# Kernel optimization log

Measured on AMD Instinct MI355X. Metric: run time of the kernel, lower is better.

## Reference

```python
import jax, jax.numpy as jnp
import numpy as np

N_NODES = 50000
N_EDGES = 640000
IN_DIM = 128
HID = 256
OUT = 256
BN_EPS = 1e-5
L2_EPS = 1e-12


def setup_inputs() -> dict:
    key = jax.random.key(0)
    ks = jax.random.split(key, 12)
    x = jax.random.normal(ks[0], (N_NODES, IN_DIM), dtype=jnp.float32)
    edge_index = jax.random.randint(ks[1], (2, N_EDGES), 0, N_NODES, dtype=jnp.int64)
    s0 = 1.0 / np.sqrt(IN_DIM)
    s1 = 1.0 / np.sqrt(HID)
    return {
        "x": x,
        "edge_index": edge_index,
        # SAGEConv layer 0: lin_l (aggregated neighbors, with bias), lin_r (root, no bias)
        "W_l0": jax.random.uniform(ks[2], (IN_DIM, HID), jnp.float32, -s0, s0),
        "b_l0": jax.random.uniform(ks[3], (HID,), jnp.float32, -s0, s0),
        "W_r0": jax.random.uniform(ks[4], (IN_DIM, HID), jnp.float32, -s0, s0),
        # SAGEConv layer 1
        "W_l1": jax.random.uniform(ks[5], (HID, OUT), jnp.float32, -s1, s1),
        "b_l1": jax.random.uniform(ks[6], (OUT,), jnp.float32, -s1, s1),
        "W_r1": jax.random.uniform(ks[7], (HID, OUT), jnp.float32, -s1, s1),
        # BatchNorm1d (eval mode: running stats)
        "bn_gamma": jax.random.uniform(ks[8], (HID,), jnp.float32, 0.5, 1.5),
        "bn_beta": 0.1 * jax.random.normal(ks[9], (HID,), dtype=jnp.float32),
        "bn_mean": 0.1 * jax.random.normal(ks[10], (HID,), dtype=jnp.float32),
        "bn_var": jax.random.uniform(ks[11], (HID,), jnp.float32, 0.5, 1.5),
    }


def _l2norm(v):
    # F.normalize(v, p=2, dim=1)
    n = jnp.sqrt(jnp.sum(v * v, axis=1, keepdims=True))
    return v / jnp.maximum(n, L2_EPS)


def _sage_mean(x, src, dst, W_l, b_l, W_r, n_nodes):
    # mean-aggregate source features at destination nodes (PyG source_to_target)
    msg = x[src]                                   # [E, d] gather
    agg = jax.ops.segment_sum(msg, dst, num_segments=n_nodes)
    cnt = jax.ops.segment_sum(jnp.ones((src.shape[0], 1), x.dtype), dst, num_segments=n_nodes)
    agg = agg / jnp.maximum(cnt, 1.0)
    out = agg @ W_l + b_l + x @ W_r
    return _l2norm(out)                            # SAGEConv(normalize=True)


def reference(x, edge_index, W_l0, b_l0, W_r0, W_l1, b_l1, W_r1,
              bn_gamma, bn_beta, bn_mean, bn_var):
    src, dst = edge_index[0], edge_index[1]
    n = x.shape[0]
    h = _sage_mean(x, src, dst, W_l0, b_l0, W_r0, n)
    # BatchNorm1d in eval mode (dropout is identity in eval)
    h = (h - bn_mean) * (bn_gamma / jnp.sqrt(bn_var + BN_EPS)) + bn_beta
    h = jax.nn.relu(h)
    h = _sage_mean(h, src, dst, W_l1, b_l1, W_r1, n)
    # final F.normalize(x, p=2, dim=1)
    return _l2norm(h)
```

## Files before the change

### kernel.cpp

```cpp
#include <hip/hip_runtime.h>

#define NN 50000

typedef __bf16 bf16x8 __attribute__((ext_vector_type(8)));
typedef float f32x4 __attribute__((ext_vector_type(4)));
typedef float f32x2 __attribute__((ext_vector_type(2)));

__device__ __forceinline__ unsigned short f2bf(float f) {
    unsigned int u = __builtin_bit_cast(unsigned int, f);
    u += 0x7FFF + ((u >> 16) & 1);
    return (unsigned short)(u >> 16);
}
__device__ __forceinline__ unsigned char f2fp8(float f) {
    return (unsigned char)(__builtin_amdgcn_cvt_pk_fp8_f32(f, f, 0, false) & 0xff);
}
__device__ __forceinline__ void gload16(const void* g, void* l) {
    __builtin_amdgcn_global_load_lds(
        (const __attribute__((address_space(1))) unsigned int*)g,
        (__attribute__((address_space(3))) unsigned int*)l, 16, 0, 0);
}

__global__ void init_kernel(const int* __restrict__ ei32, int* __restrict__ flag,
                            int* __restrict__ cnt, int n) {
    if (blockIdx.x == 0) {
        __shared__ int red[256];
        int tid = threadIdx.x;
        int o = 0;
        for (int i = tid; i < 4096; i += 256) o |= ei32[2 * i + 1];
        red[tid] = o;
        __syncthreads();
        for (int s = 128; s > 0; s >>= 1) {
            if (tid < s) red[tid] |= red[tid + s];
            __syncthreads();
        }
        if (tid == 0) *flag = (red[0] == 0) ? 1 : 0;
    } else {
        int i0 = (blockIdx.x - 1) * 1024 + threadIdx.x * 4;
#pragma unroll
        for (int j = 0; j < 4; ++j) {
            int i = i0 + j;
            if (i < n) cnt[i] = 0;
        }
    }
}

__device__ __forceinline__ int load_edge(const void* ei, int is64, long long idx) {
    return is64 ? (int)((const long long*)ei)[idx] : ((const int*)ei)[idx];
}

__global__ void hist_kernel(const void* __restrict__ ei, const int* __restrict__ flag,
                            int* __restrict__ cnt, unsigned short* __restrict__ rank, int E) {
    int e = blockIdx.x * blockDim.x + threadIdx.x;
    if (e >= E) return;
    int is64 = *flag;
    int dst = load_edge(ei, is64, (long long)E + e);
    int r = atomicAdd(&cnt[dst], 1);
    rank[e] = (unsigned short)r;
}

__global__ void scan_part(const int* __restrict__ cnt, int* __restrict__ bsum, int n) {
    __shared__ int s[256];
    const int tid = threadIdx.x;
    const int i0 = blockIdx.x * 1024 + tid * 4;
    int sum = 0;
#pragma unroll
    for (int j = 0; j < 4; ++j) {
        int i = i0 + j;
        if (i < n) sum += cnt[i];
    }
    s[tid] = sum;
    __syncthreads();
    for (int o = 128; o > 0; o >>= 1) {
        if (tid < o) s[tid] += s[tid + o];
        __syncthreads();
    }
    if (tid == 0) bsum[blockIdx.x] = s[0];
}

__global__ void scan_fin2(const int* __restrict__ cnt, const int* __restrict__ bsum,
                          int* __restrict__ off, int n, int nb) {
    __shared__ int s[256];
    __shared__ int base_sh, total_sh;
    const int tid = threadIdx.x;
    if (tid < 64) {
        int v = (tid < nb) ? bsum[tid] : 0;
        int incl = v;
#pragma unroll
        for (int o = 1; o < 64; o <<= 1) {
            int t = __shfl_up(incl, o, 64);
            if (tid >= o) incl += t;
        }
        if (tid == (int)blockIdx.x) base_sh = incl - v;
        if (tid == 63) total_sh = incl;
    }
    const int i0 = blockIdx.x * 1024 + tid * 4;
    int v[4];
    int sum = 0;
#pragma unroll
    for (int j = 0; j < 4; ++j) {
        int i = i0 + j;
        v[j] = (i < n) ? cnt[i] : 0;
        sum += v[j];
    }
    s[tid] = sum;
    __syncthreads();
    for (int o = 1; o < 256; o <<= 1) {
        int t = 0;
        if (tid >= o) t = s[tid - o];
        __syncthreads();
        s[tid] += t;
        __syncthreads();
    }
    int run = base_sh + s[tid] - sum;
#pragma unroll
    for (int j = 0; j < 4; ++j) {
        int i = i0 + j;
        if (i < n) {
            off[i] = run;
            run += v[j];
        }
    }
    if (blockIdx.x == 0 && tid == 0) off[n] = total_sh;
}

__global__ void fill_prep(const void* __restrict__ ei, const int* __restrict__ flag,
                          const int* __restrict__ off, const unsigned short* __restrict__ rank,
                          unsigned short* __restrict__ adj, int E, int EB,
                          const float* __restrict__ x, unsigned char* __restrict__ xf8,
                          unsigned short* __restrict__ xbf_t,
                          const float* __restrict__ Wl0, const float* __restrict__ Wr0,
                          unsigned short* __restrict__ Wt0,
                          const float* __restrict__ Wl1, const float* __restrict__ Wr1,
                          unsigned short* __restrict__ Wt1, int n4, int NC) {
    int b = blockIdx.x;
    if (b < EB) {
        int e = b * 256 + threadIdx.x;
        if (e >= E) return;
        int is64 = *flag;
        int src = load_edge(ei, is64, e);
        int dst = load_edge(ei, is64, (long long)E + e);
        int p = off[dst] + (int)rank[e];
        adj[p] = (unsigned short)src;
    } else if (b < EB + NC) {
        int i = (b - EB) * 256 + threadIdx.x;
        if (i >= n4) return;
        float4 v = ((const float4*)x)[i];
        int p8 = __builtin_amdgcn_cvt_pk_fp8_f32(v.x, v.y, 0, false);
        p8 = __builtin_amdgcn_cvt_pk_fp8_f32(v.z, v.w, p8, true);
        ((unsigned int*)xf8)[i] = (unsigned int)p8;
        uint2 o;
        o.x = (unsigned int)f2bf(v.x) | ((unsigned int)f2bf(v.y) << 16);
        o.y = (unsigned int)f2bf(v.z) | ((unsigned int)f2bf(v.w) << 16);
        int r = i >> 5;
        int kk = (i & 31) * 4;
        int ts = kk >> 5, q = (kk >> 3) & 3, e = kk & 7;
        size_t idx = ((size_t)(r >> 6) * 4 + ts) * 2048 + q * 512 + (r & 63) * 8 + e;
        *(uint2*)(xbf_t + idx) = o;
    } else if (b < EB + NC + 256) {
        int c = b - EB - NC;
        for (int k = threadIdx.x; k < 256; k += blockDim.x) {
            float v = (k < 128) ? Wl0[(size_t)k * 256 + c] : Wr0[(size_t)(k - 128) * 256 + c];
            int ks = k >> 5, q = (k >> 3) & 3, e = k & 7;
            Wt0[(size_t)ks * 8192 + q * 2048 + c * 8 + e] = f2bf(v);
        }
    } else {
        int c = b - EB - NC - 256;
        for (int k = threadIdx.x; k < 512; k += blockDim.x) {
            float v = (k < 256) ? Wl1[(size_t)k * 256 + c] : Wr1[(size_t)(k - 256) * 256 + c];
            int ks = k >> 5, q = (k >> 3) & 3, e = k & 7;
            Wt1[(size_t)ks * 8192 + q * 2048 + c * 8 + e] = f2bf(v);
        }
    }
}

__global__ void agg_l0(const unsigned char* __restrict__ feat8, const int* __restrict__ off,
                       const unsigned short* __restrict__ adj,
                       unsigned short* __restrict__ out_t, int n) {
    int node = blockIdx.x * 8 + (threadIdx.x >> 5);
    if (node >= n) return;
    const int lane = threadIdx.x & 31;
    const int s = off[node], e = off[node + 1];

    float a0[4] = {}, a1[4] = {}, a2[4] = {}, a3[4] = {};
    const unsigned char* fbase = feat8 + lane * 4;

    auto addrow = [&](float* acc, int src) {
        unsigned int u = *(const unsigned int*)(fbase + (size_t)src * 128);
        f32x2 lo = __builtin_amdgcn_cvt_pk_f32_fp8(u, false);
        f32x2 hi = __builtin_amdgcn_cvt_pk_f32_fp8(u, true);
        acc[0] += lo[0];
        acc[1] += lo[1];
        acc[2] += hi[0];
        acc[3] += hi[1];
    };

    int j = s;
    for (; j + 4 <= e; j += 4) {
        int i0 = adj[j], i1 = adj[j + 1], i2 = adj[j + 2], i3 = adj[j + 3];
        addrow(a0, i0);
        addrow(a1, i1);
        addrow(a2, i2);
        addrow(a3, i3);
    }
    {
        int rem = e - j;
        if (rem > 0) addrow(a0, adj[j]);
        if (rem > 1) addrow(a1, adj[j + 1]);
        if (rem > 2) addrow(a2, adj[j + 2]);
    }

    int deg = e - s;
    float inv = 1.0f / (float)(deg > 0 ? deg : 1);
#pragma unroll
    for (int k = 0; k < 4; ++k) a0[k] = (a0[k] + a1[k] + a2[k] + a3[k]) * inv;

    const int k0 = lane * 4;
    const int ts = k0 >> 5, q = (k0 >> 3) & 3, e8 = k0 & 7;
    size_t idx = ((size_t)(node >> 6) * 4 + ts) * 2048 + q * 512 + (node & 63) * 8 + e8;
    uint2 o;
    o.x = (unsigned int)f2bf(a0[0]) | ((unsigned int)f2bf(a0[1]) << 16);
    o.y = (unsigned int)f2bf(a0[2]) | ((unsigned int)f2bf(a0[3]) << 16);
    *(uint2*)(out_t + idx) = o;
}

__global__ void agg_l1(const unsigned char* __restrict__ feat8, const int* __restrict__ off,
                       const unsigned short* __restrict__ adj,
                       unsigned short* __restrict__ out_t, int n) {
    int node = blockIdx.x * 8 + (threadIdx.x >> 5);
    if (node >= n) return;
    const int lane = threadIdx.x & 31;
    const int s = off[node], e = off[node + 1];

    float a0[8] = {}, a1[8] = {}, a2[8] = {}, a3[8] = {};
    const unsigned char* fbase = feat8 + lane * 8;

    auto addrow = [&](float* acc, int src) {
        uint2 u = *(const uint2*)(fbase + (size_t)src * 256);
        f32x2 p0 = __builtin_amdgcn_cvt_pk_f32_fp8(u.x, false);
        f32x2 p1 = __builtin_amdgcn_cvt_pk_f32_fp8(u.x, true);
        f32x2 p2 = __builtin_amdgcn_cvt_pk_f32_fp8(u.y, false);
        f32x2 p3 = __builtin_amdgcn_cvt_pk_f32_fp8(u.y, true);
        acc[0] += p0[0];
        acc[1] += p0[1];
        acc[2] += p1[0];
        acc[3] += p1[1];
        acc[4] += p2[0];
        acc[5] += p2[1];
        acc[6] += p3[0];
        acc[7] += p3[1];
    };

    int j = s;
    for (; j + 4 <= e; j += 4) {
        int i0 = adj[j], i1 = adj[j + 1], i2 = adj[j + 2], i3 = adj[j + 3];
        addrow(a0, i0);
        addrow(a1, i1);
        addrow(a2, i2);
        addrow(a3, i3);
    }
    {
        int rem = e - j;
        if (rem > 0) addrow(a0, adj[j]);
        if (rem > 1) addrow(a1, adj[j + 1]);
        if (rem > 2) addrow(a2, adj[j + 2]);
    }

    int deg = e - s;
    float inv = 1.0f / (float)(deg > 0 ? deg : 1);
#pragma unroll
    for (int k = 0; k < 8; ++k) a0[k] = (a0[k] + a1[k] + a2[k] + a3[k]) * inv;

    const int k0 = lane * 8;
    const int ts = k0 >> 5, q = (k0 >> 3) & 3;
    size_t idx = ((size_t)(node >> 6) * 8 + ts) * 2048 + q * 512 + (node & 63) * 8;
    uint4 o;
    o.x = (unsigned int)f2bf(a0[0]) | ((unsigned int)f2bf(a0[1]) << 16);
    o.y = (unsigned int)f2bf(a0[2]) | ((unsigned int)f2bf(a0[3]) << 16);
    o.z = (unsigned int)f2bf(a0[4]) | ((unsigned int)f2bf(a0[5]) << 16);
    o.w = (unsigned int)f2bf(a0[6]) | ((unsigned int)f2bf(a0[7]) << 16);
    *(uint4*)(out_t + idx) = o;
}

template <int KH, bool L0>
__device__ __forceinline__ void sage_body(
    unsigned char (*a_sh)[4096], unsigned char (*b_sh)[16384],
    float (*red)[64], float* inv_sh,
    const unsigned short* __restrict__ Aagg_t, const unsigned short* __restrict__ Axin_t,
    const unsigned short* __restrict__ WtT, const float* __restrict__ bl,
    const float* __restrict__ bng, const float* __restrict__ bnb,
    const float* __restrict__ bnm, const float* __restrict__ bnv,
    unsigned char* __restrict__ hout8, unsigned short* __restrict__ hout_t,
    float* __restrict__ fout, int n) {
    constexpr int NSTEP = (2 * KH) / 32;
    constexpr int NAT = KH / 32;

    const int tid = threadIdx.x;
    const int w = tid >> 6;
    const int l = tid & 63;
    const int g = l >> 4;
    const int li = l & 15;
    const int row0 = blockIdx.x * 64;
    const int blk = blockIdx.x;

    f32x4 acc[4][4];
#pragma unroll
    for (int m = 0; m < 4; ++m)
#pragma unroll
        for (int nn = 0; nn < 4; ++nn) acc[m][nn] = (f32x4)(0.0f);

    auto stage = [&](int buf, int t) {
        const unsigned short* at =
            (t < NAT) ? Aagg_t + ((size_t)blk * NAT + t) * 2048
                      : Axin_t + ((size_t)blk * NAT + (t - NAT)) * 2048;
        gload16((const char*)at + w * 1024 + l * 16, &a_sh[buf][w * 1024]);
#pragma unroll
        for (int q = 0; q < 4; ++q)
            gload16((const char*)(WtT + (size_t)t * 8192) + q * 4096 + w * 1024 + l * 16,
                    &b_sh[buf][q * 4096 + w * 1024]);
    };

    auto compute = [&](int buf) {
        bf16x8 bfr[4];
#pragma unroll
        for (int nn = 0; nn < 4; ++nn)
            bfr[nn] = __builtin_bit_cast(
                bf16x8, *(const uint4*)&b_sh[buf][g * 4096 + (w * 64 + nn * 16 + li) * 16]);
        bf16x8 afr[4];
#pragma unroll
        for (int m = 0; m < 4; ++m)
            afr[m] = __builtin_bit_cast(bf16x8, *(const uint4*)&a_sh[buf][g * 1024 + (16 * m + li) * 16]);
#pragma unroll
        for (int nn = 0; nn < 4; ++nn)
#pragma unroll
            for (int m = 0; m < 4; ++m)
                acc[m][nn] = __builtin_amdgcn_mfma_f32_16x16x32_bf16(afr[m], bfr[nn], acc[m][nn], 0, 0, 0);
    };

    stage(0, 0);
    __syncthreads();

    int cur = 0;
    for (int ks = 0; ks < NSTEP - 1; ++ks) {
        stage(cur ^ 1, ks + 1);
        asm volatile("s_waitcnt vmcnt(5)" ::: "memory");
        __builtin_amdgcn_sched_barrier(0);
        __builtin_amdgcn_s_barrier();
        __builtin_amdgcn_sched_barrier(0);
        compute(cur);
        __builtin_amdgcn_s_barrier();
        __builtin_amdgcn_sched_barrier(0);
        cur ^= 1;
    }
    asm volatile("s_waitcnt vmcnt(0)" ::: "memory");
    __builtin_amdgcn_sched_barrier(0);
    __builtin_amdgcn_s_barrier();
    __builtin_amdgcn_sched_barrier(0);
    compute(cur);

    float bv[4];
#pragma unroll
    for (int nn = 0; nn < 4; ++nn) bv[nn] = bl[w * 64 + nn * 16 + li];
#pragma unroll
    for (int m = 0; m < 4; ++m)
#pragma unroll
        for (int nn = 0; nn < 4; ++nn)
#pragma unroll
            for (int r = 0; r < 4; ++r) acc[m][nn][r] += bv[nn];

    float ssp[4][4];
#pragma unroll
    for (int m = 0; m < 4; ++m)
#pragma unroll
        for (int r = 0; r < 4; ++r) {
            float s = 0.f;
#pragma unroll
            for (int nn = 0; nn < 4; ++nn) s += acc[m][nn][r] * acc[m][nn][r];
#pragma unroll
            for (int mk = 1; mk < 16; mk <<= 1) s += __shfl_xor(s, mk, 64);
            ssp[m][r] = s;
        }
    __syncthreads();
    if (li == 0) {
#pragma unroll
        for (int m = 0; m < 4; ++m)
#pragma unroll
            for (int r = 0; r < 4; ++r) red[w][16 * m + 4 * g + r] = ssp[m][r];
    }
    __syncthreads();
    if (tid < 64) {
        float tot = red[0][tid] + red[1][tid] + red[2][tid] + red[3][tid];
        inv_sh[tid] = 1.0f / fmaxf(sqrtf(tot), 1e-12f);
    }
    __syncthreads();

    float sc[4], sh[4];
    if (L0) {
#pragma unroll
        for (int nn = 0; nn < 4; ++nn) {
            int c = w * 64 + nn * 16 + li;
            float s = bng[c] * rsqrtf(bnv[c] + 1e-5f);
            sc[nn] = s;
            sh[nn] = bnb[c] - bnm[c] * s;
        }
    }
#pragma unroll
    for (int m = 0; m < 4; ++m) {
#pragma unroll
        for (int r = 0; r < 4; ++r) {
            int rl = 16 * m + 4 * g + r;
            int row = row0 + rl;
            if (row < n) {
                float inv = inv_sh[rl];
#pragma unroll
                for (int nn = 0; nn < 4; ++nn) {
                    int c = w * 64 + nn * 16 + li;
                    float v = acc[m][nn][r] * inv;
                    if (L0) {
                        v = fmaxf(v * sc[nn] + sh[nn], 0.f);
                        hout8[(size_t)row * 256 + c] = f2fp8(v);
                        int ts = c >> 5, q = (c >> 3) & 3, e8 = c & 7;
                        hout_t[((size_t)(row >> 6) * 8 + ts) * 2048 + q * 512 + (row & 63) * 8 + e8] =
                            f2bf(v);
                    } else {
                        fout[(size_t)row * 256 + c] = v;
                    }
                }
            }
        }
    }
}

__global__ void gemm_l0(const unsigned short* __restrict__ Aagg_t,
                        const unsigned short* __restrict__ Axin_t,
                        const unsigned short* __restrict__ WtT, const float* __restrict__ bl,
                        const float* __restrict__ bng, const float* __restrict__ bnb,
                        const float* __restrict__ bnm, const float* __restrict__ bnv,
                        unsigned char* __restrict__ hout8, unsigned short* __restrict__ hout_t,
                        int n) {
    __shared__ __align__(16) unsigned char a_sh[2][4096];
    __shared__ __align__(16) unsigned char b_sh[2][16384];
    __shared__ float red[4][64];
    __shared__ float inv_sh[64];
    sage_body<128, true>(a_sh, b_sh, red, inv_sh, Aagg_t, Axin_t, WtT, bl, bng, bnb, bnm, bnv,
                         hout8, hout_t, nullptr, n);
}

__global__ void gemm_l1(const unsigned short* __restrict__ Aagg_t,
                        const unsigned short* __restrict__ Axin_t,
                        const unsigned short* __restrict__ WtT, const float* __restrict__ bl,
                        float* __restrict__ fout, int n) {
    __shared__ __align__(16) unsigned char a_sh[2][4096];
    __shared__ __align__(16) unsigned char b_sh[2][16384];
    __shared__ float red[4][64];
    __shared__ float inv_sh[64];
    sage_body<256, false>(a_sh, b_sh, red, inv_sh, Aagg_t, Axin_t, WtT, bl, nullptr, nullptr,
                          nullptr, nullptr, nullptr, nullptr, fout, n);
}

extern "C" void kernel_launch(void* const* d_in, const int* in_sizes, int n_in,
                              void* d_out, int out_size, void* d_ws, size_t ws_size,
                              hipStream_t stream) {
    const float* x   = (const float*)d_in[0];
    const void*  ei  = d_in[1];
    const float* Wl0 = (const float*)d_in[2];
    const float* bl0 = (const float*)d_in[3];
    const float* Wr0 = (const float*)d_in[4];
    const float* Wl1 = (const float*)d_in[5];
    const float* bl1 = (const float*)d_in[6];
    const float* Wr1 = (const float*)d_in[7];
    const float* bng = (const float*)d_in[8];
    const float* bnb = (const float*)d_in[9];
    const float* bnm = (const float*)d_in[10];
    const float* bnv = (const float*)d_in[11];
    float* out = (float*)d_out;

    const int N = NN;
    const int E = in_sizes[1] / 2;
    const int NB = (N + 1023) / 1024;
    const int NBK = (N + 63) / 64;
    const int EB = (E + 255) / 256;

    char* wsp = (char*)d_ws;
    size_t o = 0;
    auto carve = [&](size_t bytes) {
        void* p = wsp + o;
        o = (o + bytes + 255) & ~(size_t)255;
        return p;
    };
    int* flag = (int*)carve(4);
    int* cnt  = (int*)carve((size_t)N * 4);
    int* off  = (int*)carve((size_t)(N + 1) * 4);
    int* bsum = (int*)carve((size_t)NB * 4);
    unsigned short* rank = (unsigned short*)carve((size_t)E * 2);
    unsigned short* adj  = (unsigned short*)carve((size_t)E * 2);
    unsigned char*  xf8  = (unsigned char*)carve((size_t)N * 128);
    unsigned char*  hf8  = (unsigned char*)carve((size_t)N * 256);
    unsigned short* big  = (unsigned short*)carve((size_t)NBK * 8 * 2048 * 2);
    unsigned short* xbf_t  = big;
    unsigned short* agg0_t = big + (size_t)NBK * 4 * 2048;
    unsigned short* agg1_t = big;
    unsigned short* hbf_t  = (unsigned short*)carve((size_t)NBK * 8 * 2048 * 2);
    unsigned short* Wt0  = (unsigned short*)carve((size_t)8 * 8192 * 2);
    unsigned short* Wt1  = (unsigned short*)carve((size_t)16 * 8192 * 2);

    init_kernel<<<1 + NB, 256, 0, stream>>>((const int*)ei, flag, cnt, N);
    hist_kernel<<<EB, 256, 0, stream>>>(ei, flag, cnt, rank, E);
    scan_part<<<NB, 256, 0, stream>>>(cnt, bsum, N);
    scan_fin2<<<NB, 256, 0, stream>>>(cnt, bsum, off, N, NB);

    const int n4 = N * 128 / 4;
    const int NC = (n4 + 255) / 256;
    fill_prep<<<EB + NC + 512, 256, 0, stream>>>(ei, flag, off, rank, adj, E, EB, x, xf8,
                                                 xbf_t, Wl0, Wr0, Wt0, Wl1, Wr1, Wt1, n4, NC);

    agg_l0<<<(N + 7) / 8, 256, 0, stream>>>(xf8, off, adj, agg0_t, N);
    gemm_l0<<<NBK, 256, 0, stream>>>(agg0_t, xbf_t, Wt0, bl0, bng, bnb, bnm, bnv,
                                     hf8, hbf_t, N);

    agg_l1<<<(N + 7) / 8, 256, 0, stream>>>(hf8, off, adj, agg1_t, N);
    gemm_l1<<<NBK, 256, 0, stream>>>(agg1_t, hbf_t, Wt1, bl1, out, N);
}
```

Before: 173.2 us.

## Double GEMM row tile to 128 and fuse the two-pass offset scan

The SAGE GEMM kernels now give each block 128 rows instead of 64. Each block stages two A row-tiles per K step and keeps 8x4 MFMA accumulators per wave, so every staged weight tile is reused across twice as many rows and total weight traffic from global memory is halved. The cost is more accumulator registers, more LDS and half as many blocks, which may lower occupancy and load balance across CUs. Separately, the two scan kernels become one: each block recomputes its own base by summing all earlier counts, trading some redundant reads for one fewer launch and the bsum buffer.

```diff
diff --git a/kernel.cpp b/kernel.cpp
--- a/kernel.cpp
+++ b/kernel.cpp
@@ -58,42 +58,22 @@
     rank[e] = (unsigned short)r;
 }
 
-__global__ void scan_part(const int* __restrict__ cnt, int* __restrict__ bsum, int n) {
+__global__ void scan_fused(const int* __restrict__ cnt, int* __restrict__ off, int n, int nb) {
     __shared__ int s[256];
     const int tid = threadIdx.x;
-    const int i0 = blockIdx.x * 1024 + tid * 4;
-    int sum = 0;
-#pragma unroll
-    for (int j = 0; j < 4; ++j) {
-        int i = i0 + j;
-        if (i < n) sum += cnt[i];
-    }
-    s[tid] = sum;
+    const int blk = blockIdx.x;
+    int lim = blk * 1024;
+    int partial = 0;
+    for (int i = tid; i < lim; i += 256) partial += cnt[i];
+    s[tid] = partial;
     __syncthreads();
     for (int o = 128; o > 0; o >>= 1) {
         if (tid < o) s[tid] += s[tid + o];
         __syncthreads();
     }
-    if (tid == 0) bsum[blockIdx.x] = s[0];
-}
-
-__global__ void scan_fin2(const int* __restrict__ cnt, const int* __restrict__ bsum,
-                          int* __restrict__ off, int n, int nb) {
-    __shared__ int s[256];
-    __shared__ int base_sh, total_sh;
-    const int tid = threadIdx.x;
-    if (tid < 64) {
-        int v = (tid < nb) ? bsum[tid] : 0;
-        int incl = v;
-#pragma unroll
-        for (int o = 1; o < 64; o <<= 1) {
-            int t = __shfl_up(incl, o, 64);
-            if (tid >= o) incl += t;
-        }
-        if (tid == (int)blockIdx.x) base_sh = incl - v;
-        if (tid == 63) total_sh = incl;
-    }
-    const int i0 = blockIdx.x * 1024 + tid * 4;
+    const int base = s[0];
+    __syncthreads();
+    const int i0 = blk * 1024 + tid * 4;
     int v[4];
     int sum = 0;
 #pragma unroll
@@ -111,7 +91,7 @@
         s[tid] += t;
         __syncthreads();
     }
-    int run = base_sh + s[tid] - sum;
+    int run = base + s[tid] - sum;
 #pragma unroll
     for (int j = 0; j < 4; ++j) {
         int i = i0 + j;
@@ -120,7 +100,7 @@
             run += v[j];
         }
     }
-    if (blockIdx.x == 0 && tid == 0) off[n] = total_sh;
+    if (blk == nb - 1 && tid == 255) off[n] = base + s[255];
 }
 
 __global__ void fill_prep(const void* __restrict__ ei, const int* __restrict__ flag,
@@ -283,8 +263,8 @@
 
 template <int KH, bool L0>
 __device__ __forceinline__ void sage_body(
-    unsigned char (*a_sh)[4096], unsigned char (*b_sh)[16384],
-    float (*red)[64], float* inv_sh,
+    unsigned char (*a_sh)[8192], unsigned char (*b_sh)[16384],
+    float (*red)[128], float* inv_sh,
     const unsigned short* __restrict__ Aagg_t, const unsigned short* __restrict__ Axin_t,
     const unsigned short* __restrict__ WtT, const float* __restrict__ bl,
     const float* __restrict__ bng, const float* __restrict__ bnb,
@@ -299,20 +279,23 @@
     const int l = tid & 63;
     const int g = l >> 4;
     const int li = l & 15;
-    const int row0 = blockIdx.x * 64;
-    const int blk = blockIdx.x;
-
-    f32x4 acc[4][4];
-#pragma unroll
-    for (int m = 0; m < 4; ++m)
+    const int row0 = blockIdx.x * 128;
+    const int rb0 = blockIdx.x * 2;
+
+    f32x4 acc[8][4];
+#pragma unroll
+    for (int m = 0; m < 8; ++m)
 #pragma unroll
         for (int nn = 0; nn < 4; ++nn) acc[m][nn] = (f32x4)(0.0f);
 
     auto stage = [&](int buf, int t) {
-        const unsigned short* at =
-            (t < NAT) ? Aagg_t + ((size_t)blk * NAT + t) * 2048
-                      : Axin_t + ((size_t)blk * NAT + (t - NAT)) * 2048;
-        gload16((const char*)at + w * 1024 + l * 16, &a_sh[buf][w * 1024]);
+        const unsigned short* base = (t < NAT) ? Aagg_t : Axin_t;
+        const int tt = (t < NAT) ? t : t - NAT;
+#pragma unroll
+        for (int h = 0; h < 2; ++h) {
+            const unsigned short* at = base + ((size_t)(rb0 + h) * NAT + tt) * 2048;
+            gload16((const char*)at + w * 1024 + l * 16, &a_sh[buf][h * 4096 + w * 1024]);
+        }
 #pragma unroll
         for (int q = 0; q < 4; ++q)
             gload16((const char*)(WtT + (size_t)t * 8192) + q * 4096 + w * 1024 + l * 16,
@@ -325,14 +308,16 @@
         for (int nn = 0; nn < 4; ++nn)
             bfr[nn] = __builtin_bit_cast(
                 bf16x8, *(const uint4*)&b_sh[buf][g * 4096 + (w * 64 + nn * 16 + li) * 16]);
-        bf16x8 afr[4];
-#pragma unroll
-        for (int m = 0; m < 4; ++m)
-            afr[m] = __builtin_bit_cast(bf16x8, *(const uint4*)&a_sh[buf][g * 1024 + (16 * m + li) * 16]);
+        bf16x8 afr[8];
+#pragma unroll
+        for (int m = 0; m < 8; ++m)
+            afr[m] = __builtin_bit_cast(
+                bf16x8,
+                *(const uint4*)&a_sh[buf][(m >> 2) * 4096 + g * 1024 + (16 * (m & 3) + li) * 16]);
 #pragma unroll
         for (int nn = 0; nn < 4; ++nn)
 #pragma unroll
-            for (int m = 0; m < 4; ++m)
+            for (int m = 0; m < 8; ++m)
                 acc[m][nn] = __builtin_amdgcn_mfma_f32_16x16x32_bf16(afr[m], bfr[nn], acc[m][nn], 0, 0, 0);
     };
 
@@ -342,7 +327,7 @@
     int cur = 0;
     for (int ks = 0; ks < NSTEP - 1; ++ks) {
         stage(cur ^ 1, ks + 1);
-        asm volatile("s_waitcnt vmcnt(5)" ::: "memory");
+        asm volatile("s_waitcnt vmcnt(6)" ::: "memory");
         __builtin_amdgcn_sched_barrier(0);
         __builtin_amdgcn_s_barrier();
         __builtin_amdgcn_sched_barrier(0);
@@ -361,15 +346,15 @@
 #pragma unroll
     for (int nn = 0; nn < 4; ++nn) bv[nn] = bl[w * 64 + nn * 16 + li];
 #pragma unroll
-    for (int m = 0; m < 4; ++m)
+    for (int m = 0; m < 8; ++m)
 #pragma unroll
         for (int nn = 0; nn < 4; ++nn)
 #pragma unroll
             for (int r = 0; r < 4; ++r) acc[m][nn][r] += bv[nn];
 
-    float ssp[4][4];
-#pragma unroll
-    for (int m = 0; m < 4; ++m)
+    float ssp[8][4];
+#pragma unroll
+    for (int m = 0; m < 8; ++m)
 #pragma unroll
         for (int r = 0; r < 4; ++r) {
             float s = 0.f;
@@ -382,12 +367,13 @@
     __syncthreads();
     if (li == 0) {
 #pragma unroll
-        for (int m = 0; m < 4; ++m)
-#pragma unroll
-            for (int r = 0; r < 4; ++r) red[w][16 * m + 4 * g + r] = ssp[m][r];
-    }
-    __syncthreads();
-    if (tid < 64) {
+        for (int m = 0; m < 8; ++m)
+#pragma unroll
+            for (int r = 0; r < 4; ++r)
+                red[w][(m >> 2) * 64 + 16 * (m & 3) + 4 * g + r] = ssp[m][r];
+    }
+    __syncthreads();
+    if (tid < 128) {
         float tot = red[0][tid] + red[1][tid] + red[2][tid] + red[3][tid];
         inv_sh[tid] = 1.0f / fmaxf(sqrtf(tot), 1e-12f);
     }
@@ -404,10 +390,10 @@
         }
     }
 #pragma unroll
-    for (int m = 0; m < 4; ++m) {
+    for (int m = 0; m < 8; ++m) {
 #pragma unroll
         for (int r = 0; r < 4; ++r) {
-            int rl = 16 * m + 4 * g + r;
+            int rl = (m >> 2) * 64 + 16 * (m & 3) + 4 * g + r;
             int row = row0 + rl;
             if (row < n) {
                 float inv = inv_sh[rl];
@@ -437,10 +423,10 @@
                         const float* __restrict__ bnm, const float* __restrict__ bnv,
                         unsigned char* __restrict__ hout8, unsigned short* __restrict__ hout_t,
                         int n) {
-    __shared__ __align__(16) unsigned char a_sh[2][4096];
+    __shared__ __align__(16) unsigned char a_sh[2][8192];
     __shared__ __align__(16) unsigned char b_sh[2][16384];
-    __shared__ float red[4][64];
-    __shared__ float inv_sh[64];
+    __shared__ float red[4][128];
+    __shared__ float inv_sh[128];
     sage_body<128, true>(a_sh, b_sh, red, inv_sh, Aagg_t, Axin_t, WtT, bl, bng, bnb, bnm, bnv,
                          hout8, hout_t, nullptr, n);
 }
@@ -449,10 +435,10 @@
                         const unsigned short* __restrict__ Axin_t,
                         const unsigned short* __restrict__ WtT, const float* __restrict__ bl,
                         float* __restrict__ fout, int n) {
-    __shared__ __align__(16) unsigned char a_sh[2][4096];
+    __shared__ __align__(16) unsigned char a_sh[2][8192];
     __shared__ __align__(16) unsigned char b_sh[2][16384];
-    __shared__ float red[4][64];
-    __shared__ float inv_sh[64];
+    __shared__ float red[4][128];
+    __shared__ float inv_sh[128];
     sage_body<256, false>(a_sh, b_sh, red, inv_sh, Aagg_t, Axin_t, WtT, bl, nullptr, nullptr,
                           nullptr, nullptr, nullptr, nullptr, fout, n);
 }
@@ -478,6 +464,7 @@
     const int E = in_sizes[1] / 2;
     const int NB = (N + 1023) / 1024;
     const int NBK = (N + 63) / 64;
+    const int NG = (N + 127) / 128;
     const int EB = (E + 255) / 256;
 
     char* wsp = (char*)d_ws;
@@ -490,7 +477,6 @@
     int* flag = (int*)carve(4);
     int* cnt  = (int*)carve((size_t)N * 4);
     int* off  = (int*)carve((size_t)(N + 1) * 4);
-    int* bsum = (int*)carve((size_t)NB * 4);
     unsigned short* rank = (unsigned short*)carve((size_t)E * 2);
     unsigned short* adj  = (unsigned short*)carve((size_t)E * 2);
     unsigned char*  xf8  = (unsigned char*)carve((size_t)N * 128);
@@ -505,8 +491,7 @@
 
     init_kernel<<<1 + NB, 256, 0, stream>>>((const int*)ei, flag, cnt, N);
     hist_kernel<<<EB, 256, 0, stream>>>(ei, flag, cnt, rank, E);
-    scan_part<<<NB, 256, 0, stream>>>(cnt, bsum, N);
-    scan_fin2<<<NB, 256, 0, stream>>>(cnt, bsum, off, N, NB);
+    scan_fused<<<NB, 256, 0, stream>>>(cnt, off, N, NB);
 
     const int n4 = N * 128 / 4;
     const int NC = (n4 + 255) / 256;
@@ -514,9 +499,9 @@
                                                  xbf_t, Wl0, Wr0, Wt0, Wl1, Wr1, Wt1, n4, NC);
 
     agg_l0<<<(N + 7) / 8, 256, 0, stream>>>(xf8, off, adj, agg0_t, N);
-    gemm_l0<<<NBK, 256, 0, stream>>>(agg0_t, xbf_t, Wt0, bl0, bng, bnb, bnm, bnv,
-                                     hf8, hbf_t, N);
+    gemm_l0<<<NG, 256, 0, stream>>>(agg0_t, xbf_t, Wt0, bl0, bng, bnb, bnm, bnv,
+                                    hf8, hbf_t, N);
 
     agg_l1<<<(N + 7) / 8, 256, 0, stream>>>(hf8, off, adj, agg1_t, N);
-    gemm_l1<<<NBK, 256, 0, stream>>>(agg1_t, hbf_t, Wt1, bl1, out, N);
-}
+    gemm_l1<<<NG, 256, 0, stream>>>(agg1_t, hbf_t, Wt1, bl1, out, N);
+}
```

New measurement: 390.7 us. 2.26x slower.
